# Kernel optimization log

Measured on AMD Instinct MI355X. Metric: run time of the kernel, lower is better.

The kernel has to match this reference:

```python
import jax, jax.numpy as jnp
import numpy as np

EPS = 1e-5  # BatchNorm eps (torch default)


def point_sample(feat, points):
    """Bilinear sample feat [B,C,Hf,Wf] at points [B,K,2] (x,y in [0,1]),
    matching F.grid_sample(2*p-1, mode='bilinear', padding_mode='zeros',
    align_corners=False)."""
    B, C, Hf, Wf = feat.shape
    x = points[..., 0] * Wf - 0.5  # [B,K] pixel coords
    y = points[..., 1] * Hf - 0.5
    x0f = jnp.floor(x); y0f = jnp.floor(y)
    wx = (x - x0f)[:, None, :]  # [B,1,K]
    wy = (y - y0f)[:, None, :]
    x0 = x0f.astype(jnp.int32); y0 = y0f.astype(jnp.int32)
    flat = feat.reshape(B, C, Hf * Wf)

    def gather(xi, yi):
        valid = ((xi >= 0) & (xi < Wf) & (yi >= 0) & (yi < Hf))[:, None, :]
        lin = jnp.clip(yi, 0, Hf - 1) * Wf + jnp.clip(xi, 0, Wf - 1)  # [B,K]
        idx = jnp.broadcast_to(lin[:, None, :], (B, C, lin.shape[1]))
        return jnp.take_along_axis(flat, idx, axis=2) * valid

    v00 = gather(x0, y0)
    v10 = gather(x0 + 1, y0)
    v01 = gather(x0, y0 + 1)
    v11 = gather(x0 + 1, y0 + 1)
    return (v00 * (1 - wx) * (1 - wy) + v10 * wx * (1 - wy)
            + v01 * (1 - wx) * wy + v11 * wx * wy)


def bn(x, g, b, m, v):
    # eval-mode BatchNorm1d over channel dim of [B,C,K]
    scale = (g / jnp.sqrt(v + EPS))[None, :, None]
    return (x - m[None, :, None]) * scale + b[None, :, None]


def setup_inputs() -> dict:
    key = jax.random.key(0)
    ks = jax.random.split(key, 20)
    B, H, W = 8, 512, 512
    Cf = 256
    d = {
        'uncertainty_map': jax.random.normal(ks[0], (B, 1, H, W), jnp.float32),
        'prev_mask': jax.random.uniform(ks[1], (B, 1, H, W), jnp.float32),
        'enc_f': jax.random.normal(ks[2], (B, Cf, 128, 128), jnp.float32),
        'w1': jax.random.normal(ks[3], (256, Cf + 1), jnp.float32) * 0.05,
        'b1': jax.random.normal(ks[4], (256,), jnp.float32) * 0.05,
        'g1': jnp.ones((256,), jnp.float32),
        'be1': jnp.zeros((256,), jnp.float32),
        'm1': jax.random.normal(ks[5], (256,), jnp.float32) * 0.1,
        'v1': jax.random.uniform(ks[6], (256,), jnp.float32) + 0.5,
        'w2': jax.random.normal(ks[7], (256, 256), jnp.float32) * 0.05,
        'b2': jax.random.normal(ks[8], (256,), jnp.float32) * 0.05,
        'g2': jnp.ones((256,), jnp.float32),
        'be2': jnp.zeros((256,), jnp.float32),
        'm2': jax.random.normal(ks[9], (256,), jnp.float32) * 0.1,
        'v2': jax.random.uniform(ks[10], (256,), jnp.float32) + 0.5,
        'w3': jax.random.normal(ks[11], (1, 256), jnp.float32) * 0.05,
        'b3': jax.random.normal(ks[12], (1,), jnp.float32) * 0.05,
    }
    return d


def reference(uncertainty_map, prev_mask, enc_f,
              w1, b1, g1, be1, m1, v1,
              w2, b2, g2, be2, m2, v2,
              w3, b3):
    B, C, H, W = prev_mask.shape
    K = H * W // 10
    # K least-uncertain points (topk largest=False)
    _, idx = jax.lax.top_k(-uncertainty_map.reshape(B, -1), K)  # [B,K] int32
    col = (idx % W).astype(jnp.float32)
    row = (idx // W).astype(jnp.float32)
    points = jnp.stack([(col + 0.5) / W, (row + 0.5) / H], axis=-1)  # [B,K,2]

    coarse = point_sample(prev_mask, points)  # [B,1,K]
    fine = point_sample(enc_f, points)        # [B,Cf,K]
    h = jnp.concatenate([coarse, fine], axis=1)  # [B,Cf+1,K]

    h = jax.nn.relu(bn(jnp.einsum('oc,bck->bok', w1, h) + b1[None, :, None], g1, be1, m1, v1))
    h = jax.nn.relu(bn(jnp.einsum('oc,bck->bok', w2, h) + b2[None, :, None], g2, be2, m2, v2))
    refined = jax.nn.sigmoid(jnp.einsum('oc,bck->bok', w3, h) + b3[None, :, None])  # [B,1,K]

    flat = prev_mask.reshape(B, C, H * W)
    bi = jnp.arange(B)[:, None, None]
    ci = jnp.arange(C)[None, :, None]
    out = flat.at[bi, ci, idx[:, None, :]].set(jnp.broadcast_to(refined, (B, C, K)))
    return out.reshape(B, C, H, W)
```

## Files before the change

### kernel.cpp

```cpp
#include <hip/hip_runtime.h>
#include <hip/hip_bf16.h>

#define HW_IMG 262144
#define KSEL   26214
#define NB     8
#define CF     256
#define LDW1   288
#define LDACT  296

typedef short    short8 __attribute__((ext_vector_type(8)));
typedef float    f32x4  __attribute__((ext_vector_type(4)));
typedef unsigned u32x2  __attribute__((ext_vector_type(2)));
typedef unsigned short u16x4 __attribute__((ext_vector_type(4)));

__device__ __forceinline__ unsigned f2key(float f){
    unsigned u = __builtin_bit_cast(unsigned, f);
    return (u & 0x80000000u) ? ~u : (u | 0x80000000u);
}
__device__ __forceinline__ unsigned short f2bf(float f){
    unsigned u = __builtin_bit_cast(unsigned, f);
    u = u + 0x7FFFu + ((u >> 16) & 1u);
    return (unsigned short)(u >> 16);
}
__device__ __forceinline__ float bf2f(unsigned short s){
    unsigned u = ((unsigned)s) << 16;
    return __builtin_bit_cast(float, u);
}

__global__ __launch_bounds__(256) void k_prep(
    const float* __restrict__ w1, const float* __restrict__ w2,
    const float* __restrict__ b1, const float* __restrict__ g1, const float* __restrict__ be1,
    const float* __restrict__ m1, const float* __restrict__ v1,
    const float* __restrict__ b2, const float* __restrict__ g2, const float* __restrict__ be2,
    const float* __restrict__ m2, const float* __restrict__ v2,
    unsigned short* __restrict__ w1p, unsigned short* __restrict__ w2p,
    float* __restrict__ c1, float* __restrict__ c2)
{
    int tid = blockIdx.x * 256 + threadIdx.x;
    if (tid < 256 * LDW1) {
        int o = tid / LDW1, k = tid % LDW1;
        float scale = g1[o] * rsqrtf(v1[o] + 1e-5f);
        float val = 0.f;
        if (k < 256) val = w1[o * 257 + k + 1];
        else if (k == 256) val = w1[o * 257];
        w1p[tid] = f2bf(val * scale);
        if (k == 0) c1[o] = (b1[o] - m1[o]) * scale + be1[o];
    } else {
        int t2 = tid - 256 * LDW1;
        if (t2 < 65536) {
            int o = t2 >> 8;
            float scale = g2[o] * rsqrtf(v2[o] + 1e-5f);
            w2p[t2] = f2bf(w2[t2] * scale);
            if ((t2 & 255) == 0) c2[o] = (b2[o] - m2[o]) * scale + be2[o];
        }
    }
}

__global__ __launch_bounds__(256) void k_transpose(
    const float* __restrict__ enc, unsigned short* __restrict__ encT)
{
    __shared__ __align__(16) unsigned short tile[64][72];
    int b = blockIdx.z;
    int pixbase = blockIdx.x * 64;
    int chbase  = blockIdx.y * 64;
    int t = threadIdx.x;
    int pix = t & 63, cg = t >> 6;
    const float* src = enc + (size_t)b * CF * 16384;
#pragma unroll
    for (int i = 0; i < 16; i++) {
        int c = chbase + cg * 16 + i;
        tile[pix][cg * 16 + i] = f2bf(src[(size_t)c * 16384 + pixbase + pix]);
    }
    __syncthreads();
    unsigned short* dst = encT + (size_t)b * 16384 * CF;
#pragma unroll
    for (int pass = 0; pass < 4; pass++) {
        int pl = pass * 16 + (t >> 4);
        int c4 = (t & 15) * 4;
        *(u16x4*)(dst + (size_t)(pixbase + pl) * CF + chbase + c4) = *(const u16x4*)&tile[pl][c4];
    }
}


__global__ __launch_bounds__(256) void k_histA(const float* __restrict__ unc, unsigned* __restrict__ hist)
{
    __shared__ unsigned lh[4][4096];
    int b = blockIdx.y, t = threadIdx.x;
    int wv = t >> 6;
    for (int i = t; i < 4 * 4096; i += 256) ((unsigned*)lh)[i] = 0;
    __syncthreads();
    const float4* src = (const float4*)(unc + (size_t)b * HW_IMG + blockIdx.x * 4096);
    unsigned* mine = lh[wv];
#pragma unroll
    for (int j = 0; j < 4; j++) {
        float4 v = src[j * 256 + t];
        atomicAdd(&mine[f2key(v.x) >> 20], 1u);
        atomicAdd(&mine[f2key(v.y) >> 20], 1u);
        atomicAdd(&mine[f2key(v.z) >> 20], 1u);
        atomicAdd(&mine[f2key(v.w) >> 20], 1u);
    }
    __syncthreads();
    unsigned* gh = hist + (size_t)b * 4096;
    for (int i = t; i < 4096; i += 256) {
        unsigned c = lh[0][i] + lh[1][i] + lh[2][i] + lh[3][i];
        if (c) atomicAdd(&gh[i], c);
    }
}

__global__ __launch_bounds__(256) void k_histB(const float* __restrict__ unc,
    const unsigned* __restrict__ meta, unsigned* __restrict__ hist)
{
    __shared__ unsigned lh[4096];
    int b = blockIdx.y, t = threadIdx.x;
    unsigned binA = meta[b * 8 + 0];
    for (int i = t; i < 4096; i += 256) lh[i] = 0;
    __syncthreads();
    const float4* src = (const float4*)(unc + (size_t)b * HW_IMG + blockIdx.x * 4096);
#pragma unroll
    for (int j = 0; j < 4; j++) {
        float4 v = src[j * 256 + t];
        unsigned k;
        k = f2key(v.x); if ((k >> 20) == binA) atomicAdd(&lh[(k >> 8) & 0xFFFu], 1u);
        k = f2key(v.y); if ((k >> 20) == binA) atomicAdd(&lh[(k >> 8) & 0xFFFu], 1u);
        k = f2key(v.z); if ((k >> 20) == binA) atomicAdd(&lh[(k >> 8) & 0xFFFu], 1u);
        k = f2key(v.w); if ((k >> 20) == binA) atomicAdd(&lh[(k >> 8) & 0xFFFu], 1u);
    }
    __syncthreads();
    unsigned* gh = hist + (size_t)b * 4096;
    for (int i = t; i < 4096; i += 256) { unsigned c = lh[i]; if (c) atomicAdd(&gh[i], c); }
}

__global__ __launch_bounds__(256) void k_histC(const float* __restrict__ unc,
    const unsigned* __restrict__ meta, unsigned* __restrict__ hist)
{
    __shared__ unsigned lh[256];
    int b = blockIdx.y, t = threadIdx.x;
    unsigned pre24 = (meta[b * 8 + 0] << 12) | meta[b * 8 + 2];
    lh[t] = 0;
    __syncthreads();
    const float4* src = (const float4*)(unc + (size_t)b * HW_IMG + blockIdx.x * 4096);
#pragma unroll
    for (int j = 0; j < 4; j++) {
        float4 v = src[j * 256 + t];
        unsigned k;
        k = f2key(v.x); if ((k >> 8) == pre24) atomicAdd(&lh[k & 0xFFu], 1u);
        k = f2key(v.y); if ((k >> 8) == pre24) atomicAdd(&lh[k & 0xFFu], 1u);
        k = f2key(v.z); if ((k >> 8) == pre24) atomicAdd(&lh[k & 0xFFu], 1u);
        k = f2key(v.w); if ((k >> 8) == pre24) atomicAdd(&lh[k & 0xFFu], 1u);
    }
    __syncthreads();
    unsigned* gh = hist + (size_t)b * 4096;
    unsigned c = lh[t];
    if (c) atomicAdd(&gh[t], c);
}

__global__ __launch_bounds__(256) void k_find(const unsigned* __restrict__ hist,
    unsigned* __restrict__ meta, int per, int stage)
{
    int b = blockIdx.x, t = threadIdx.x;
    const unsigned* h = hist + (size_t)b * 4096;
    unsigned base = (stage == 0) ? 0u : meta[b * 8 + 2 * stage - 1];
    __shared__ unsigned seg[256], pref[256];
    unsigned s = 0;
    for (int i = 0; i < per; i++) s += h[t * per + i];
    seg[t] = s;
    __syncthreads();
    if (t == 0) { unsigned c = base; for (int i = 0; i < 256; i++) { pref[i] = c; c += seg[i]; } }
    __syncthreads();
    if (pref[t] < KSEL && KSEL <= pref[t] + seg[t]) {
        unsigned c = pref[t];
        for (int i = 0; i < per; i++) {
            unsigned cnt = h[t * per + i];
            if (c + cnt >= KSEL) {
                unsigned bin = (unsigned)(t * per + i);
                meta[b * 8 + 2 * stage] = bin;
                meta[b * 8 + 2 * stage + 1] = c;
                if (stage == 2)
                    meta[b * 8 + 6] = (meta[b * 8 + 0] << 20) | (meta[b * 8 + 2] << 8) | bin;
                break;
            }
            c += cnt;
        }
    }
}

__global__ __launch_bounds__(256) void k_count(const float* __restrict__ unc,
    const unsigned* __restrict__ meta, unsigned* __restrict__ cntL, unsigned* __restrict__ cntE)
{
    int b = blockIdx.y, blk = blockIdx.x, t = threadIdx.x;
    unsigned pivot = meta[b * 8 + 6];
    const float4* src = (const float4*)(unc + (size_t)b * HW_IMG + blk * 1024);
    float4 v = src[t];
    unsigned k0 = f2key(v.x), k1 = f2key(v.y), k2 = f2key(v.z), k3 = f2key(v.w);
    unsigned cl = (k0 < pivot) + (k1 < pivot) + (k2 < pivot) + (k3 < pivot);
    unsigned ce = (k0 == pivot) + (k1 == pivot) + (k2 == pivot) + (k3 == pivot);
    __shared__ unsigned rl[256], re[256];
    rl[t] = cl; re[t] = ce; __syncthreads();
    for (int s = 128; s > 0; s >>= 1) { if (t < s) { rl[t] += rl[t + s]; re[t] += re[t + s]; } __syncthreads(); }
    if (t == 0) { cntL[b * 256 + blk] = rl[0]; cntE[b * 256 + blk] = re[0]; }
}

__global__ void k_scan(const unsigned* __restrict__ cntL, const unsigned* __restrict__ cntE,
                       unsigned* __restrict__ offL, unsigned* __restrict__ offE)
{
    int b = blockIdx.x;
    if (threadIdx.x == 0) {
        unsigned c = 0;
        for (int i = 0; i < 256; i++) { offL[b * 256 + i] = c; c += cntL[b * 256 + i]; }
        c = 0;
        for (int i = 0; i < 256; i++) { offE[b * 256 + i] = c; c += cntE[b * 256 + i]; }
    }
}

__global__ __launch_bounds__(256) void k_emit(const float* __restrict__ unc,
    const unsigned* __restrict__ meta, const unsigned* __restrict__ offL,
    const unsigned* __restrict__ offE, unsigned* __restrict__ sel)
{
    int b = blockIdx.y, blk = blockIdx.x, t = threadIdx.x;
    unsigned pivot = meta[b * 8 + 6], cless = meta[b * 8 + 5], r = KSEL - cless;
    int base = blk * 1024 + t * 4;
    const float4* src = (const float4*)(unc + (size_t)b * HW_IMG + blk * 1024);
    float4 v = src[t];
    unsigned key[4] = { f2key(v.x), f2key(v.y), f2key(v.z), f2key(v.w) };
    unsigned cl = 0, ce = 0;
#pragma unroll
    for (int j = 0; j < 4; j++) { cl += (key[j] < pivot); ce += (key[j] == pivot); }
    __shared__ unsigned sL[256], sE[256];
    sL[t] = cl; sE[t] = ce; __syncthreads();
    for (int off = 1; off < 256; off <<= 1) {
        unsigned aL = (t >= off) ? sL[t - off] : 0u;
        unsigned aE = (t >= off) ? sE[t - off] : 0u;
        __syncthreads();
        sL[t] += aL; sE[t] += aE;
        __syncthreads();
    }
    unsigned posL = offL[b * 256 + blk] + sL[t] - cl;
    unsigned posE = offE[b * 256 + blk] + sE[t] - ce;
    unsigned* sb = sel + (size_t)b * KSEL;
#pragma unroll
    for (int j = 0; j < 4; j++) {
        if (key[j] < pivot) { sb[posL++] = (unsigned)(base + j); }
        else if (key[j] == pivot) { if (posE < r) sb[cless + posE] = (unsigned)(base + j); posE++; }
    }
}

__global__ __launch_bounds__(256, 2) void k_main(
    const unsigned* __restrict__ sel, const float* __restrict__ prev,
    const unsigned short* __restrict__ encT,
    const unsigned short* __restrict__ w1p, const unsigned short* __restrict__ w2p,
    const float* __restrict__ c1, const float* __restrict__ c2,
    const float* __restrict__ w3, const float* __restrict__ b3,
    float* __restrict__ out)
{
    __shared__ __align__(16) unsigned short act[64][LDACT];
    __shared__ unsigned sIdx[64];
    __shared__ float sPart[4][64];

    int b = blockIdx.y;
    int pbase = blockIdx.x * 64;
    int npts = KSEL - pbase; if (npts > 64) npts = 64;
    int t = threadIdx.x;

    if (t < 64) {
        unsigned id = (t < npts) ? sel[(size_t)b * KSEL + pbase + t] : 0u;
        sIdx[t] = id;
        act[t][256] = f2bf(prev[(size_t)b * HW_IMG + id]);
#pragma unroll
        for (int k = 257; k < LDW1; k++) act[t][k] = 0;
    }
    __syncthreads();

    {
        int wv = t >> 6, l = t & 63;
        int g = l >> 2, sub = l & 3;
        int p = wv * 16 + g;
        unsigned id = sIdx[p];
        int col = id & 511, row = (int)(id >> 9);
        float xf = (col - 1.5f) * 0.25f;
        float yf = (row - 1.5f) * 0.25f;
        float x0f = floorf(xf), y0f = floorf(yf);
        int x0 = (int)x0f, y0 = (int)y0f;
        float wx = xf - x0f, wy = yf - y0f;
        float wxa = (x0 >= 0) ? (1.f - wx) : 0.f;
        float wxb = (x0 <= 126) ? wx : 0.f;
        float wya = (y0 >= 0) ? (1.f - wy) : 0.f;
        float wyb = (y0 <= 126) ? wy : 0.f;
        int xc0 = x0 < 0 ? 0 : x0;
        int xc1 = (x0 + 1 > 127) ? 127 : x0 + 1;
        int yc0 = y0 < 0 ? 0 : y0;
        int yc1 = (y0 + 1 > 127) ? 127 : y0 + 1;
        float w00 = wxa * wya, w10 = wxb * wya, w01 = wxa * wyb, w11 = wxb * wyb;
        const unsigned short* bb = encT + (size_t)b * 16384 * CF + sub * 64;
        const unsigned short* p00 = bb + (size_t)(yc0 * 128 + xc0) * CF;
        const unsigned short* p10 = bb + (size_t)(yc0 * 128 + xc1) * CF;
        const unsigned short* p01 = bb + (size_t)(yc1 * 128 + xc0) * CF;
        const unsigned short* p11 = bb + (size_t)(yc1 * 128 + xc1) * CF;
#pragma unroll 2
        for (int ch = 0; ch < 8; ch++) {
            short8 va = *(const short8*)(p00 + ch * 8);
            short8 vb = *(const short8*)(p10 + ch * 8);
            short8 vc = *(const short8*)(p01 + ch * 8);
            short8 vd = *(const short8*)(p11 + ch * 8);
            short8 rr;
#pragma unroll
            for (int j = 0; j < 8; j++) {
                float f = w00 * bf2f((unsigned short)va[j]) + w10 * bf2f((unsigned short)vb[j])
                        + w01 * bf2f((unsigned short)vc[j]) + w11 * bf2f((unsigned short)vd[j]);
                rr[j] = (short)f2bf(f);
            }
            *(short8*)&act[p][sub * 64 + ch * 8] = rr;
        }
    }
    __syncthreads();

    int wv = t >> 6, l = t & 63;
    int lr = l & 15, lk = l >> 4;
    f32x4 acc[4][4];
#pragma unroll
    for (int m = 0; m < 4; m++)
#pragma unroll
        for (int n = 0; n < 4; n++) acc[m][n] = (f32x4){0.f, 0.f, 0.f, 0.f};

#pragma unroll
    for (int kk = 0; kk < 9; kk++) {
        int k0 = kk * 32 + lk * 8;
        short8 afr[4], bfr[4];
#pragma unroll
        for (int m = 0; m < 4; m++)
            afr[m] = *(const short8*)(w1p + (size_t)(wv * 64 + m * 16 + lr) * LDW1 + k0);
#pragma unroll
        for (int n = 0; n < 4; n++)
            bfr[n] = *(const short8*)&act[n * 16 + lr][k0];
#pragma unroll
        for (int m = 0; m < 4; m++)
#pragma unroll
            for (int n = 0; n < 4; n++)
                acc[m][n] = __builtin_amdgcn_mfma_f32_16x16x32_bf16(afr[m], bfr[n], acc[m][n], 0, 0, 0);
    }
    __syncthreads();

#pragma unroll
    for (int m = 0; m < 4; m++) {
        int chb = wv * 64 + m * 16 + lk * 4;
        float c0 = c1[chb], cA = c1[chb + 1], cB = c1[chb + 2], cC = c1[chb + 3];
#pragma unroll
        for (int n = 0; n < 4; n++) {
            int p = n * 16 + lr;
            float v0 = fmaxf(acc[m][n][0] + c0, 0.f);
            float v1 = fmaxf(acc[m][n][1] + cA, 0.f);
            float v2 = fmaxf(acc[m][n][2] + cB, 0.f);
            float v3 = fmaxf(acc[m][n][3] + cC, 0.f);
            u32x2 pk;
            pk[0] = (unsigned)f2bf(v0) | ((unsigned)f2bf(v1) << 16);
            pk[1] = (unsigned)f2bf(v2) | ((unsigned)f2bf(v3) << 16);
            *(u32x2*)&act[p][chb] = pk;
        }
    }
    __syncthreads();

#pragma unroll
    for (int m = 0; m < 4; m++)
#pragma unroll
        for (int n = 0; n < 4; n++) acc[m][n] = (f32x4){0.f, 0.f, 0.f, 0.f};
#pragma unroll
    for (int kk = 0; kk < 8; kk++) {
        int k0 = kk * 32 + lk * 8;
        short8 afr[4], bfr[4];
#pragma unroll
        for (int m = 0; m < 4; m++)
            afr[m] = *(const short8*)(w2p + (size_t)(wv * 64 + m * 16 + lr) * 256 + k0);
#pragma unroll
        for (int n = 0; n < 4; n++)
            bfr[n] = *(const short8*)&act[n * 16 + lr][k0];
#pragma unroll
        for (int m = 0; m < 4; m++)
#pragma unroll
            for (int n = 0; n < 4; n++)
                acc[m][n] = __builtin_amdgcn_mfma_f32_16x16x32_bf16(afr[m], bfr[n], acc[m][n], 0, 0, 0);
    }

    float part[4] = {0.f, 0.f, 0.f, 0.f};
#pragma unroll
    for (int m = 0; m < 4; m++) {
        int chb = wv * 64 + m * 16 + lk * 4;
#pragma unroll
        for (int r = 0; r < 4; r++) {
            float wr = w3[chb + r];
            float cr = c2[chb + r];
#pragma unroll
            for (int n = 0; n < 4; n++)
                part[n] += wr * fmaxf(acc[m][n][r] + cr, 0.f);
        }
    }
#pragma unroll
    for (int n = 0; n < 4; n++) {
        part[n] += __shfl_xor(part[n], 16);
        part[n] += __shfl_xor(part[n], 32);
    }
    if (lk == 0) {
#pragma unroll
        for (int n = 0; n < 4; n++) sPart[wv][n * 16 + lr] = part[n];
    }
    __syncthreads();
    if (t < 64) {
        float tot = sPart[0][t] + sPart[1][t] + sPart[2][t] + sPart[3][t] + b3[0];
        float refined = 1.f / (1.f + __expf(-tot));
        if (t < npts) out[(size_t)b * HW_IMG + sIdx[t]] = refined;
    }
}

extern "C" void kernel_launch(void* const* d_in, const int* in_sizes, int n_in,
                              void* d_out, int out_size, void* d_ws, size_t ws_size,
                              hipStream_t stream)
{
    (void)in_sizes; (void)n_in; (void)out_size; (void)ws_size;
    const float* unc  = (const float*)d_in[0];
    const float* prev = (const float*)d_in[1];
    const float* enc  = (const float*)d_in[2];
    const float* w1   = (const float*)d_in[3];
    const float* b1   = (const float*)d_in[4];
    const float* g1   = (const float*)d_in[5];
    const float* be1  = (const float*)d_in[6];
    const float* m1   = (const float*)d_in[7];
    const float* v1   = (const float*)d_in[8];
    const float* w2   = (const float*)d_in[9];
    const float* b2   = (const float*)d_in[10];
    const float* g2   = (const float*)d_in[11];
    const float* be2  = (const float*)d_in[12];
    const float* m2   = (const float*)d_in[13];
    const float* v2   = (const float*)d_in[14];
    const float* w3   = (const float*)d_in[15];
    const float* b3   = (const float*)d_in[16];
    float* out = (float*)d_out;

    char* ws = (char*)d_ws;
    size_t off = 0;
    auto alloc = [&](size_t bytes) { size_t o = off; off += (bytes + 255) & ~(size_t)255; return o; };
    size_t o_encT = alloc((size_t)NB * 16384 * CF * 2);
    size_t o_w1p  = alloc((size_t)256 * LDW1 * 2);
    size_t o_w2p  = alloc((size_t)256 * 256 * 2);
    size_t o_c1   = alloc(256 * 4);
    size_t o_c2   = alloc(256 * 4);
    size_t o_hist = alloc((size_t)3 * NB * 4096 * 4);
    size_t o_meta = alloc(NB * 8 * 4);
    size_t o_cntL = alloc(NB * 256 * 4);
    size_t o_cntE = alloc(NB * 256 * 4);
    size_t o_offL = alloc(NB * 256 * 4);
    size_t o_offE = alloc(NB * 256 * 4);
    size_t o_sel  = alloc((size_t)NB * KSEL * 4);

    unsigned short* encT = (unsigned short*)(ws + o_encT);
    unsigned short* w1p  = (unsigned short*)(ws + o_w1p);
    unsigned short* w2p  = (unsigned short*)(ws + o_w2p);
    float* c1p = (float*)(ws + o_c1);
    float* c2p = (float*)(ws + o_c2);
    unsigned* histA = (unsigned*)(ws + o_hist);
    unsigned* histB = histA + (size_t)NB * 4096;
    unsigned* histC = histB + (size_t)NB * 4096;
    unsigned* meta  = (unsigned*)(ws + o_meta);
    unsigned* cntL  = (unsigned*)(ws + o_cntL);
    unsigned* cntE  = (unsigned*)(ws + o_cntE);
    unsigned* offL  = (unsigned*)(ws + o_offL);
    unsigned* offE  = (unsigned*)(ws + o_offE);
    unsigned* sel   = (unsigned*)(ws + o_sel);

    hipMemsetAsync(ws + o_hist, 0, (size_t)3 * NB * 4096 * 4, stream);
    hipMemcpyAsync(d_out, (const void*)prev, (size_t)NB * HW_IMG * 4, hipMemcpyDeviceToDevice, stream);

    k_prep<<<544, 256, 0, stream>>>(w1, w2, b1, g1, be1, m1, v1, b2, g2, be2, m2, v2,
                                    w1p, w2p, c1p, c2p);
    k_transpose<<<dim3(256, 4, NB), 256, 0, stream>>>(enc, encT);

    k_histA<<<dim3(64, NB), 256, 0, stream>>>(unc, histA);
    k_find <<<NB, 256, 0, stream>>>(histA, meta, 16, 0);
    k_histB<<<dim3(64, NB), 256, 0, stream>>>(unc, meta, histB);
    k_find <<<NB, 256, 0, stream>>>(histB, meta, 16, 1);
    k_histC<<<dim3(64, NB), 256, 0, stream>>>(unc, meta, histC);
    k_find <<<NB, 256, 0, stream>>>(histC, meta, 1, 2);
    k_count<<<dim3(256, NB), 256, 0, stream>>>(unc, meta, cntL, cntE);
    k_scan <<<NB, 64, 0, stream>>>(cntL, cntE, offL, offE);
    k_emit <<<dim3(256, NB), 256, 0, stream>>>(unc, meta, offL, offE, sel);

    k_main<<<dim3((KSEL + 63) / 64, NB), 256, 0, stream>>>(sel, prev, encT, w1p, w2p,
                                                           c1p, c2p, w3, b3, out);
}
```

Before: 244.8 us.

## Split fused gather+MLP kernel into separate gather and MLP kernels with swizzled LDS

Splits the single main kernel into a bilinear-gather kernel that writes sampled bf16 features to a padded global buffer and an MLP kernel that loads them with coalesced reads. The split is meant to let the latency-bound random gathers run at full occupancy, separate from the MFMA phase, which now targets higher occupancy (launch bounds 4). It also adds an XOR swizzle on LDS activation columns to reduce bank conflicts, and interleaves the batch index across block IDs. The cost is an extra global round trip of about 107 MB of intermediate data plus one more kernel launch.

```diff
diff --git a/kernel.cpp b/kernel.cpp
--- a/kernel.cpp
+++ b/kernel.cpp
@@ -7,6 +7,10 @@
 #define CF     256
 #define LDW1   288
 #define LDACT  296
+#define NBLK_MAIN 410
+#define NPTS_PAD 26240
+
+#define ACOL(c) ((c) ^ ((((c) >> 6) & 3) << 4))
 
 typedef short    short8 __attribute__((ext_vector_type(8)));
 typedef float    f32x4  __attribute__((ext_vector_type(4)));
@@ -244,72 +248,95 @@
     }
 }
 
-__global__ __launch_bounds__(256, 2) void k_main(
+__global__ __launch_bounds__(256) void k_gather(
+    const unsigned* __restrict__ sel, const unsigned short* __restrict__ encT,
+    unsigned short* __restrict__ gout)
+{
+    int wg = blockIdx.x;
+    int b  = wg & 7;
+    int pbase = (wg >> 3) * 64;
+    int t = threadIdx.x;
+    const unsigned* selb = sel + (size_t)b * KSEL;
+
+    int wv2 = t >> 6, l2 = t & 63;
+    int g = l2 >> 2, sub = l2 & 3;
+    int p = wv2 * 16 + g;
+    int gi = pbase + p; if (gi >= KSEL) gi = KSEL - 1;
+    unsigned id = selb[gi];
+    int col = id & 511, row = (int)(id >> 9);
+    float xf = (col - 1.5f) * 0.25f;
+    float yf = (row - 1.5f) * 0.25f;
+    float x0f = floorf(xf), y0f = floorf(yf);
+    int x0 = (int)x0f, y0 = (int)y0f;
+    float wx = xf - x0f, wy = yf - y0f;
+    float wxa = (x0 >= 0) ? (1.f - wx) : 0.f;
+    float wxb = (x0 <= 126) ? wx : 0.f;
+    float wya = (y0 >= 0) ? (1.f - wy) : 0.f;
+    float wyb = (y0 <= 126) ? wy : 0.f;
+    int xc0 = x0 < 0 ? 0 : x0;
+    int xc1 = (x0 + 1 > 127) ? 127 : x0 + 1;
+    int yc0 = y0 < 0 ? 0 : y0;
+    int yc1 = (y0 + 1 > 127) ? 127 : y0 + 1;
+    float w00 = wxa * wya, w10 = wxb * wya, w01 = wxa * wyb, w11 = wxb * wyb;
+    const unsigned short* bb = encT + (size_t)b * 16384 * CF + sub * 64;
+    const unsigned short* p00 = bb + (size_t)(yc0 * 128 + xc0) * CF;
+    const unsigned short* p10 = bb + (size_t)(yc0 * 128 + xc1) * CF;
+    const unsigned short* p01 = bb + (size_t)(yc1 * 128 + xc0) * CF;
+    const unsigned short* p11 = bb + (size_t)(yc1 * 128 + xc1) * CF;
+    unsigned short* dst = gout + ((size_t)b * NPTS_PAD + pbase + p) * CF + sub * 64;
+#pragma unroll 4
+    for (int ch = 0; ch < 8; ch++) {
+        short8 va = *(const short8*)(p00 + ch * 8);
+        short8 vb = *(const short8*)(p10 + ch * 8);
+        short8 vc = *(const short8*)(p01 + ch * 8);
+        short8 vd = *(const short8*)(p11 + ch * 8);
+        short8 rr;
+#pragma unroll
+        for (int j = 0; j < 8; j++) {
+            float f = w00 * bf2f((unsigned short)va[j]) + w10 * bf2f((unsigned short)vb[j])
+                    + w01 * bf2f((unsigned short)vc[j]) + w11 * bf2f((unsigned short)vd[j]);
+            rr[j] = (short)f2bf(f);
+        }
+        *(short8*)(dst + ch * 8) = rr;
+    }
+}
+
+__global__ __launch_bounds__(256, 4) void k_mlp(
     const unsigned* __restrict__ sel, const float* __restrict__ prev,
-    const unsigned short* __restrict__ encT,
+    const unsigned short* __restrict__ gout,
     const unsigned short* __restrict__ w1p, const unsigned short* __restrict__ w2p,
     const float* __restrict__ c1, const float* __restrict__ c2,
     const float* __restrict__ w3, const float* __restrict__ b3,
     float* __restrict__ out)
 {
     __shared__ __align__(16) unsigned short act[64][LDACT];
-    __shared__ unsigned sIdx[64];
     __shared__ float sPart[4][64];
 
-    int b = blockIdx.y;
-    int pbase = blockIdx.x * 64;
+    int wg = blockIdx.x;
+    int b  = wg & 7;
+    int pbase = (wg >> 3) * 64;
     int npts = KSEL - pbase; if (npts > 64) npts = 64;
     int t = threadIdx.x;
-
+    const unsigned* selb = sel + (size_t)b * KSEL;
+
+    const unsigned short* src = gout + ((size_t)b * NPTS_PAD + pbase) * CF;
+#pragma unroll
+    for (int i = 0; i < 8; i++) {
+        int e = i * 2048 + t * 8;
+        short8 v = *(const short8*)(src + e);
+        int pp = e >> 8, c = e & 255;
+        *(short8*)&act[pp][ACOL(c)] = v;
+    }
     if (t < 64) {
-        unsigned id = (t < npts) ? sel[(size_t)b * KSEL + pbase + t] : 0u;
-        sIdx[t] = id;
-        act[t][256] = f2bf(prev[(size_t)b * HW_IMG + id]);
-#pragma unroll
-        for (int k = 257; k < LDW1; k++) act[t][k] = 0;
-    }
-    __syncthreads();
-
-    {
-        int wv = t >> 6, l = t & 63;
-        int g = l >> 2, sub = l & 3;
-        int p = wv * 16 + g;
-        unsigned id = sIdx[p];
-        int col = id & 511, row = (int)(id >> 9);
-        float xf = (col - 1.5f) * 0.25f;
-        float yf = (row - 1.5f) * 0.25f;
-        float x0f = floorf(xf), y0f = floorf(yf);
-        int x0 = (int)x0f, y0 = (int)y0f;
-        float wx = xf - x0f, wy = yf - y0f;
-        float wxa = (x0 >= 0) ? (1.f - wx) : 0.f;
-        float wxb = (x0 <= 126) ? wx : 0.f;
-        float wya = (y0 >= 0) ? (1.f - wy) : 0.f;
-        float wyb = (y0 <= 126) ? wy : 0.f;
-        int xc0 = x0 < 0 ? 0 : x0;
-        int xc1 = (x0 + 1 > 127) ? 127 : x0 + 1;
-        int yc0 = y0 < 0 ? 0 : y0;
-        int yc1 = (y0 + 1 > 127) ? 127 : y0 + 1;
-        float w00 = wxa * wya, w10 = wxb * wya, w01 = wxa * wyb, w11 = wxb * wyb;
-        const unsigned short* bb = encT + (size_t)b * 16384 * CF + sub * 64;
-        const unsigned short* p00 = bb + (size_t)(yc0 * 128 + xc0) * CF;
-        const unsigned short* p10 = bb + (size_t)(yc0 * 128 + xc1) * CF;
-        const unsigned short* p01 = bb + (size_t)(yc1 * 128 + xc0) * CF;
-        const unsigned short* p11 = bb + (size_t)(yc1 * 128 + xc1) * CF;
-#pragma unroll 2
-        for (int ch = 0; ch < 8; ch++) {
-            short8 va = *(const short8*)(p00 + ch * 8);
-            short8 vb = *(const short8*)(p10 + ch * 8);
-            short8 vc = *(const short8*)(p01 + ch * 8);
-            short8 vd = *(const short8*)(p11 + ch * 8);
-            short8 rr;
-#pragma unroll
-            for (int j = 0; j < 8; j++) {
-                float f = w00 * bf2f((unsigned short)va[j]) + w10 * bf2f((unsigned short)vb[j])
-                        + w01 * bf2f((unsigned short)vc[j]) + w11 * bf2f((unsigned short)vd[j]);
-                rr[j] = (short)f2bf(f);
-            }
-            *(short8*)&act[p][sub * 64 + ch * 8] = rr;
-        }
+        int gi = pbase + t; if (gi >= KSEL) gi = KSEL - 1;
+        unsigned id = selb[gi];
+        float cv = prev[(size_t)b * HW_IMG + id];
+        short8 z = {0,0,0,0,0,0,0,0};
+        short8 c8 = z; c8[0] = (short)f2bf(cv);
+        *(short8*)&act[t][256] = c8;
+        *(short8*)&act[t][264] = z;
+        *(short8*)&act[t][272] = z;
+        *(short8*)&act[t][280] = z;
     }
     __syncthreads();
 
@@ -324,13 +351,14 @@
 #pragma unroll
     for (int kk = 0; kk < 9; kk++) {
         int k0 = kk * 32 + lk * 8;
+        int k0s = ACOL(k0);
         short8 afr[4], bfr[4];
 #pragma unroll
         for (int m = 0; m < 4; m++)
             afr[m] = *(const short8*)(w1p + (size_t)(wv * 64 + m * 16 + lr) * LDW1 + k0);
 #pragma unroll
         for (int n = 0; n < 4; n++)
-            bfr[n] = *(const short8*)&act[n * 16 + lr][k0];
+            bfr[n] = *(const short8*)&act[n * 16 + lr][k0s];
 #pragma unroll
         for (int m = 0; m < 4; m++)
 #pragma unroll
@@ -342,6 +370,7 @@
 #pragma unroll
     for (int m = 0; m < 4; m++) {
         int chb = wv * 64 + m * 16 + lk * 4;
+        int chbs = ACOL(chb);
         float c0 = c1[chb], cA = c1[chb + 1], cB = c1[chb + 2], cC = c1[chb + 3];
 #pragma unroll
         for (int n = 0; n < 4; n++) {
@@ -353,7 +382,7 @@
             u32x2 pk;
             pk[0] = (unsigned)f2bf(v0) | ((unsigned)f2bf(v1) << 16);
             pk[1] = (unsigned)f2bf(v2) | ((unsigned)f2bf(v3) << 16);
-            *(u32x2*)&act[p][chb] = pk;
+            *(u32x2*)&act[p][chbs] = pk;
         }
     }
     __syncthreads();
@@ -365,13 +394,14 @@
 #pragma unroll
     for (int kk = 0; kk < 8; kk++) {
         int k0 = kk * 32 + lk * 8;
+        int k0s = ACOL(k0);
         short8 afr[4], bfr[4];
 #pragma unroll
         for (int m = 0; m < 4; m++)
             afr[m] = *(const short8*)(w2p + (size_t)(wv * 64 + m * 16 + lr) * 256 + k0);
 #pragma unroll
         for (int n = 0; n < 4; n++)
-            bfr[n] = *(const short8*)&act[n * 16 + lr][k0];
+            bfr[n] = *(const short8*)&act[n * 16 + lr][k0s];
 #pragma unroll
         for (int m = 0; m < 4; m++)
 #pragma unroll
@@ -402,10 +432,11 @@
         for (int n = 0; n < 4; n++) sPart[wv][n * 16 + lr] = part[n];
     }
     __syncthreads();
-    if (t < 64) {
+    if (t < 64 && t < npts) {
         float tot = sPart[0][t] + sPart[1][t] + sPart[2][t] + sPart[3][t] + b3[0];
         float refined = 1.f / (1.f + __expf(-tot));
-        if (t < npts) out[(size_t)b * HW_IMG + sIdx[t]] = refined;
+        unsigned id = selb[pbase + t];
+        out[(size_t)b * HW_IMG + id] = refined;
     }
 }
 
@@ -437,6 +468,7 @@
     size_t off = 0;
     auto alloc = [&](size_t bytes) { size_t o = off; off += (bytes + 255) & ~(size_t)255; return o; };
     size_t o_encT = alloc((size_t)NB * 16384 * CF * 2);
+    size_t o_gout = alloc((size_t)NB * NPTS_PAD * CF * 2);
     size_t o_w1p  = alloc((size_t)256 * LDW1 * 2);
     size_t o_w2p  = alloc((size_t)256 * 256 * 2);
     size_t o_c1   = alloc(256 * 4);
@@ -450,6 +482,7 @@
     size_t o_sel  = alloc((size_t)NB * KSEL * 4);
 
     unsigned short* encT = (unsigned short*)(ws + o_encT);
+    unsigned short* goutp= (unsigned short*)(ws + o_gout);
     unsigned short* w1p  = (unsigned short*)(ws + o_w1p);
     unsigned short* w2p  = (unsigned short*)(ws + o_w2p);
     float* c1p = (float*)(ws + o_c1);
@@ -481,6 +514,7 @@
     k_scan <<<NB, 64, 0, stream>>>(cntL, cntE, offL, offE);
     k_emit <<<dim3(256, NB), 256, 0, stream>>>(unc, meta, offL, offE, sel);
 
-    k_main<<<dim3((KSEL + 63) / 64, NB), 256, 0, stream>>>(sel, prev, encT, w1p, w2p,
-                                                           c1p, c2p, w3, b3, out);
-}
+    k_gather<<<NBLK_MAIN * NB, 256, 0, stream>>>(sel, encT, goutp);
+    k_mlp   <<<NBLK_MAIN * NB, 256, 0, stream>>>(sel, prev, goutp, w1p, w2p,
+                                                 c1p, c2p, w3, b3, out);
+}
```

Result: slower. 323.0 us (+32.0%).
